# Optimization experiments

Measured on AMD Instinct MI355X. Metric: run time of the kernel, lower is better.

Reference implementation:

```python
import jax, jax.numpy as jnp
import numpy as np

LN_EPS = 1e-5


def setup_inputs() -> dict:
    key = jax.random.key(0)
    ks = jax.random.split(key, 8)
    N, H, E, D, B = 262144, 768, 768, 2048, 65536
    return {
        "u_t": jax.random.normal(ks[0], (B, E), dtype=jnp.float32),
        "s_i": jax.random.randint(ks[1], (B,), 0, N, dtype=jnp.int64),
        "speaker_embeddings": jax.random.normal(ks[2], (N, H), dtype=jnp.float32),
        "W1": jax.random.normal(ks[3], (D, H + E), dtype=jnp.float32) * 0.02,
        "b1": jax.random.normal(ks[4], (D,), dtype=jnp.float32) * 0.02,
        "W2": jax.random.normal(ks[5], (H, D), dtype=jnp.float32) * 0.02,
        "b2": jax.random.normal(ks[6], (H,), dtype=jnp.float32) * 0.02,
        "ln_gamma": jnp.ones((H,), dtype=jnp.float32),
        "ln_beta": jnp.zeros((H,), dtype=jnp.float32),
    }


def reference(u_t, s_i, speaker_embeddings, W1, b1, W2, b2, ln_gamma, ln_beta):
    # gather speaker vectors: [B, H]
    h_t = speaker_embeddings[s_i]
    # concat [u_t, h_t] along features: [B, E+H]
    x = jnp.concatenate([u_t, h_t], axis=-1)
    # Linear -> GELU (exact, torch default) -> (Dropout=identity in eval)
    h = jax.nn.gelu(jnp.einsum("bf,df->bd", x, W1) + b1, approximate=False)
    # Linear -> (Dropout=identity) : [B, H]
    y = jnp.einsum("bd,hd->bh", h, W2) + b2
    # LayerNorm over last dim
    mu = jnp.mean(y, axis=-1, keepdims=True)
    var = jnp.mean((y - mu) ** 2, axis=-1, keepdims=True)
    new_h_t = (y - mu) * jax.lax.rsqrt(var + LN_EPS) * ln_gamma + ln_beta
    # scatter-add back into the memory table (duplicates accumulate)
    updated = speaker_embeddings.at[s_i].add(new_h_t)
    return new_h_t, updated
```

## Files before the change

### kernel.cpp

```cpp
#include <hip/hip_runtime.h>
#include <hip/hip_bf16.h>

typedef unsigned short u16;
typedef unsigned int u32;
typedef short bf16x8 __attribute__((ext_vector_type(8)));
typedef float f32x4 __attribute__((ext_vector_type(4)));

#define BAR() asm volatile("s_barrier" ::: "memory")
#define WAITV4() asm volatile("s_waitcnt vmcnt(4)" ::: "memory")
#define WAITV0() asm volatile("s_waitcnt vmcnt(0)" ::: "memory")
#define WAITL4() asm volatile("s_waitcnt lgkmcnt(4)" ::: "memory")
#define WAITL() asm volatile("s_waitcnt lgkmcnt(0)" ::: "memory")
#define SCHED() __builtin_amdgcn_sched_barrier(0)

__device__ __forceinline__ unsigned pk2(float lo, float hi) {
    unsigned a = (unsigned)__builtin_bit_cast(u16, __float2bfloat16(lo));
    unsigned b = (unsigned)__builtin_bit_cast(u16, __float2bfloat16(hi));
    return a | (b << 16);
}
__device__ __forceinline__ u16 f2bf(float v) {
    return __builtin_bit_cast(u16, __float2bfloat16(v));
}
__device__ __forceinline__ void gl_lds16(const u16* g, u16* l) {
    __builtin_amdgcn_global_load_lds(
        (const __attribute__((address_space(1))) u32*)g,
        (__attribute__((address_space(3))) u32*)l, 16, 0, 0);
}

__global__ void cvtbf(const float4* __restrict__ s, uint2* __restrict__ d, int n4) {
    int i = blockIdx.x * blockDim.x + threadIdx.x;
    int stride = gridDim.x * blockDim.x;
    for (; i < n4; i += stride) {
        float4 f = s[i];
        uint2 o;
        o.x = pk2(f.x, f.y);
        o.y = pk2(f.z, f.w);
        d[i] = o;
    }
}

__global__ __launch_bounds__(256) void xbuild(const float* __restrict__ u_t,
                                              const float* __restrict__ emb,
                                              const int* __restrict__ s_i,
                                              u16* __restrict__ xb) {
    const long u = (long)blockIdx.x * blockDim.x + threadIdx.x;
    const int row = (int)(u / 192);
    const int c8 = (int)(u % 192);
    const float* src = (c8 < 96) ? (u_t + (long)row * 768 + c8 * 8)
                                 : (emb + (long)s_i[row] * 768 + (c8 - 96) * 8);
    float4 f0 = ((const float4*)src)[0];
    float4 f1 = ((const float4*)src)[1];
    uint4 o;
    o.x = pk2(f0.x, f0.y);
    o.y = pk2(f0.z, f0.w);
    o.z = pk2(f1.x, f1.y);
    o.w = pk2(f1.z, f1.w);
    *(uint4*)(xb + u * 8) = o;
}

template <int LDK, int NT, int TN, int EPI>
__global__ __launch_bounds__(512, 1) void gemm256(
    const u16* __restrict__ Ag, const u16* __restrict__ Bg,
    const float* __restrict__ bias, u16* __restrict__ outb,
    float* __restrict__ outf) {
    __shared__ __align__(16) u16 lds[65536];

    const int tid = threadIdx.x;
    const int lane = tid & 63;
    const int wv = tid >> 6;
    const int wm = wv >> 2;
    const int wn = wv & 3;

    const int cpx = (int)gridDim.x >> 3;
    const int tile = ((int)blockIdx.x & 7) * cpx + ((int)blockIdx.x >> 3);
    const int tm = tile / TN, tn = tile % TN;
    const long rowBase = (long)tm * 256;
    const long colBase = (long)tn * 256;

    const int srow = tid >> 2;
    const int gch = (tid & 3) ^ ((tid >> 3) & 3);
    const u16* pA = Ag + (rowBase + srow) * (long)LDK + gch * 8;
    const u16* pB = Bg + (colBase + srow) * (long)LDK + gch * 8;
    const int dstBase = wv * 512;

    auto stageA = [&](int kt, int ks, int b) {
        const u16* s = pA + kt * 64 + ks * 32;
        u16* d = lds + b * 32768 + ks * 8192 + dstBase;
        gl_lds16(s, d);
        gl_lds16(s + (long)128 * LDK, d + 4096);
    };
    auto stageB = [&](int kt, int ks, int b) {
        const u16* s = pB + kt * 64 + ks * 32;
        u16* d = lds + b * 32768 + 16384 + ks * 8192 + dstBase;
        gl_lds16(s, d);
        gl_lds16(s + (long)128 * LDK, d + 4096);
    };

    const int l15 = lane & 15, lc = lane >> 4;
    int offA[8], offB[4];
#pragma unroll
    for (int i = 0; i < 8; ++i) {
        int r = wm * 128 + i * 16 + l15;
        offA[i] = r * 32 + ((lc ^ ((r >> 1) & 3)) << 3);
    }
#pragma unroll
    for (int n = 0; n < 4; ++n) {
        int r = wn * 64 + n * 16 + l15;
        offB[n] = r * 32 + ((lc ^ ((r >> 1) & 3)) << 3);
    }

    f32x4 acc[8][4];
    const f32x4 zero = {0.f, 0.f, 0.f, 0.f};
#pragma unroll
    for (int m = 0; m < 8; ++m)
#pragma unroll
        for (int n = 0; n < 4; ++n) acc[m][n] = zero;

    stageA(0, 0, 0);
    stageB(0, 0, 0);
    stageA(0, 1, 0);
    stageB(0, 1, 0);
    WAITV4();
    BAR();

    for (int kt = 0; kt < NT; ++kt) {
        const int b = kt & 1;
        const u16* base = lds + b * 32768;
        const bool pf = (kt + 1 < NT);

#pragma unroll
        for (int ph = 0; ph < 2; ++ph) {
            const u16* rA = base + ph * 8192;
            const u16* rB = base + 16384 + ph * 8192;
            bf16x8 xB[4], xA0[4], xA1[4];
#pragma unroll
            for (int n = 0; n < 4; ++n) xB[n] = *(const bf16x8*)(rB + offB[n]);
            SCHED();
#pragma unroll
            for (int m = 0; m < 4; ++m) xA0[m] = *(const bf16x8*)(rA + offA[m]);
            SCHED();
#pragma unroll
            for (int m = 0; m < 4; ++m) xA1[m] = *(const bf16x8*)(rA + offA[4 + m]);
            SCHED();
            if (pf) { stageA(kt + 1, ph, b ^ 1); stageB(kt + 1, ph, b ^ 1); }
            BAR();
            WAITL4();
            SCHED();
            __builtin_amdgcn_s_setprio(1);
#pragma unroll
            for (int m = 0; m < 4; ++m)
#pragma unroll
                for (int n = 0; n < 4; ++n)
                    acc[m][n] = __builtin_amdgcn_mfma_f32_16x16x32_bf16(xA0[m], xB[n], acc[m][n], 0, 0, 0);
            SCHED();
            WAITL();
            SCHED();
#pragma unroll
            for (int m = 0; m < 4; ++m)
#pragma unroll
                for (int n = 0; n < 4; ++n)
                    acc[4 + m][n] = __builtin_amdgcn_mfma_f32_16x16x32_bf16(xA1[m], xB[n], acc[4 + m][n], 0, 0, 0);
            __builtin_amdgcn_s_setprio(0);
            if (pf) { WAITV4(); } else { WAITV0(); }
            BAR();
        }
    }

    const int N = TN * 256;
#pragma unroll
    for (int n = 0; n < 4; ++n) {
        long gc = colBase + wn * 64 + n * 16 + l15;
        float bv = bias[gc];
#pragma unroll
        for (int i = 0; i < 8; ++i) {
            long gr = rowBase + wm * 128 + i * 16 + (lc << 2);
#pragma unroll
            for (int j = 0; j < 4; ++j) {
                float v = acc[i][n][j] + bv;
                if constexpr (EPI == 0) {
                    float w = v * v;
                    float z = v * fmaf(w, -0.0713548162f, -1.5957691216f);
                    v = __fdividef(v, 1.0f + __expf(z));
                    outb[(gr + j) * N + gc] = f2bf(v);
                } else {
                    outf[(gr + j) * N + gc] = v;
                }
            }
        }
    }
}

__global__ __launch_bounds__(256) void ln_scatter(float* __restrict__ y,
                                                  const float* __restrict__ gamma,
                                                  const float* __restrict__ beta,
                                                  const int* __restrict__ s_i,
                                                  float* __restrict__ upd) {
    const int lane = threadIdx.x & 63;
    const long row = (long)blockIdx.x * 4 + (threadIdx.x >> 6);
    const long base = row * 768;
    float v[12];
#pragma unroll
    for (int i = 0; i < 12; ++i) v[i] = y[base + i * 64 + lane];
    float s = 0.f, q = 0.f;
#pragma unroll
    for (int i = 0; i < 12; ++i) { s += v[i]; q += v[i] * v[i]; }
#pragma unroll
    for (int off = 32; off > 0; off >>= 1) {
        s += __shfl_xor(s, off, 64);
        q += __shfl_xor(q, off, 64);
    }
    const float mu = s * (1.f / 768.f);
    const float var = q * (1.f / 768.f) - mu * mu;
    const float inv = rsqrtf(var + 1e-5f);
    const long si = s_i[row];
#pragma unroll
    for (int i = 0; i < 12; ++i) {
        int c = i * 64 + lane;
        float r = (v[i] - mu) * inv * gamma[c] + beta[c];
        y[base + c] = r;
        atomicAdd(&upd[si * 768 + c], r);
    }
}

__global__ void copy4(const float4* __restrict__ s, float4* __restrict__ d, long n) {
    long i = (long)blockIdx.x * blockDim.x + threadIdx.x;
    long stride = (long)gridDim.x * blockDim.x;
    for (; i < n; i += stride) d[i] = s[i];
}

extern "C" void kernel_launch(void* const* d_in, const int* in_sizes, int n_in,
                              void* d_out, int out_size, void* d_ws, size_t ws_size,
                              hipStream_t stream) {
    const float* u_t = (const float*)d_in[0];
    const int* s_i = (const int*)d_in[1];
    const float* emb = (const float*)d_in[2];
    const float* W1 = (const float*)d_in[3];
    const float* b1 = (const float*)d_in[4];
    const float* W2 = (const float*)d_in[5];
    const float* b2 = (const float*)d_in[6];
    const float* gamma = (const float*)d_in[7];
    const float* beta = (const float*)d_in[8];

    float* out = (float*)d_out;
    float* newh = out;
    float* upd = out + 50331648L;

    u16* base = (u16*)upd;
    u16* xb = base;
    u16* w1b = base + 100663296L;
    u16* hbuf = base + 103809024L;
    u16* w2b = base + 238026752L;

    cvtbf<<<1024, 256, 0, stream>>>((const float4*)W1, (uint2*)w1b, 786432);
    cvtbf<<<1024, 256, 0, stream>>>((const float4*)W2, (uint2*)w2b, 393216);
    xbuild<<<49152, 256, 0, stream>>>(u_t, emb, s_i, xb);
    gemm256<1536, 24, 8, 0><<<2048, 512, 0, stream>>>(xb, w1b, b1, hbuf, nullptr);
    gemm256<2048, 32, 3, 1><<<768, 512, 0, stream>>>(hbuf, w2b, b2, nullptr, newh);
    copy4<<<2048, 256, 0, stream>>>((const float4*)emb, (float4*)upd, 50331648L);
    ln_scatter<<<16384, 256, 0, stream>>>(newh, gamma, beta, s_i, upd);
}
```

Baseline: 1.369 ms.

## Simplify GEMM pipeline to whole-tile prefetch and request two blocks per CU

Restructures the GEMM main loop so the next K-tile is prefetched in full at the top of each iteration, followed by a single wait and barrier, then two sub-steps of LDS reads and MFMAs. This drops the hand-interleaved phase schedule with its sched_barriers, lgkmcnt waits and setprio. It also changes launch bounds to ask for two 512-thread blocks per CU. However, the kernel already uses 128KB of static LDS, so a second block likely cannot fit, and the register cap may cause spills of the 128-float accumulator. The simpler schedule also loses the fine-grained overlap of LDS reads with MFMA work.

```diff
diff --git a/kernel.cpp b/kernel.cpp
--- a/kernel.cpp
+++ b/kernel.cpp
@@ -7,11 +7,8 @@
 typedef float f32x4 __attribute__((ext_vector_type(4)));
 
 #define BAR() asm volatile("s_barrier" ::: "memory")
-#define WAITV4() asm volatile("s_waitcnt vmcnt(4)" ::: "memory")
+#define WAITV8() asm volatile("s_waitcnt vmcnt(8)" ::: "memory")
 #define WAITV0() asm volatile("s_waitcnt vmcnt(0)" ::: "memory")
-#define WAITL4() asm volatile("s_waitcnt lgkmcnt(4)" ::: "memory")
-#define WAITL() asm volatile("s_waitcnt lgkmcnt(0)" ::: "memory")
-#define SCHED() __builtin_amdgcn_sched_barrier(0)
 
 __device__ __forceinline__ unsigned pk2(float lo, float hi) {
     unsigned a = (unsigned)__builtin_bit_cast(u16, __float2bfloat16(lo));
@@ -59,7 +56,7 @@
 }
 
 template <int LDK, int NT, int TN, int EPI>
-__global__ __launch_bounds__(512, 1) void gemm256(
+__global__ __launch_bounds__(512, 2) void gemm256(
     const u16* __restrict__ Ag, const u16* __restrict__ Bg,
     const float* __restrict__ bias, u16* __restrict__ outb,
     float* __restrict__ outf) {
@@ -120,50 +117,36 @@
     stageB(0, 0, 0);
     stageA(0, 1, 0);
     stageB(0, 1, 0);
-    WAITV4();
-    BAR();
 
     for (int kt = 0; kt < NT; ++kt) {
         const int b = kt & 1;
-        const u16* base = lds + b * 32768;
         const bool pf = (kt + 1 < NT);
 
-#pragma unroll
-        for (int ph = 0; ph < 2; ++ph) {
-            const u16* rA = base + ph * 8192;
-            const u16* rB = base + 16384 + ph * 8192;
-            bf16x8 xB[4], xA0[4], xA1[4];
+        if (pf) {
+            stageA(kt + 1, 0, b ^ 1);
+            stageB(kt + 1, 0, b ^ 1);
+            stageA(kt + 1, 1, b ^ 1);
+            stageB(kt + 1, 1, b ^ 1);
+        }
+        if (pf) { WAITV8(); } else { WAITV0(); }
+        BAR();
+
+#pragma unroll
+        for (int kk = 0; kk < 2; ++kk) {
+            const u16* rA = lds + b * 32768 + kk * 8192;
+            const u16* rB = lds + b * 32768 + 16384 + kk * 8192;
+            bf16x8 xA[8], xB[4];
 #pragma unroll
             for (int n = 0; n < 4; ++n) xB[n] = *(const bf16x8*)(rB + offB[n]);
-            SCHED();
-#pragma unroll
-            for (int m = 0; m < 4; ++m) xA0[m] = *(const bf16x8*)(rA + offA[m]);
-            SCHED();
-#pragma unroll
-            for (int m = 0; m < 4; ++m) xA1[m] = *(const bf16x8*)(rA + offA[4 + m]);
-            SCHED();
-            if (pf) { stageA(kt + 1, ph, b ^ 1); stageB(kt + 1, ph, b ^ 1); }
-            BAR();
-            WAITL4();
-            SCHED();
-            __builtin_amdgcn_s_setprio(1);
-#pragma unroll
-            for (int m = 0; m < 4; ++m)
+#pragma unroll
+            for (int m = 0; m < 8; ++m) xA[m] = *(const bf16x8*)(rA + offA[m]);
+#pragma unroll
+            for (int m = 0; m < 8; ++m)
 #pragma unroll
                 for (int n = 0; n < 4; ++n)
-                    acc[m][n] = __builtin_amdgcn_mfma_f32_16x16x32_bf16(xA0[m], xB[n], acc[m][n], 0, 0, 0);
-            SCHED();
-            WAITL();
-            SCHED();
-#pragma unroll
-            for (int m = 0; m < 4; ++m)
-#pragma unroll
-                for (int n = 0; n < 4; ++n)
-                    acc[4 + m][n] = __builtin_amdgcn_mfma_f32_16x16x32_bf16(xA1[m], xB[n], acc[4 + m][n], 0, 0, 0);
-            __builtin_amdgcn_s_setprio(0);
-            if (pf) { WAITV4(); } else { WAITV0(); }
-            BAR();
+                    acc[m][n] = __builtin_amdgcn_mfma_f32_16x16x32_bf16(xA[m], xB[n], acc[m][n], 0, 0, 0);
         }
+        BAR();
     }
 
     const int N = TN * 256;
```

Result: slower. 1.460 ms (+6.6%).
